# Kernel optimization log

Measured on AMD Instinct MI355X. Metric: run time of the kernel, lower is better.

The kernel has to match this reference:

```python
import jax, jax.numpy as jnp
import numpy as np

B, L, H = 2, 2048, 1024
NH = 4
K = int(H * 0.5)       # key_dim = 512
V = int(H * 1.0)       # value_dim = 1024
DK, DV = K // NH, V // NH   # 128, 256
PR = 32                # proj_low_rank_dim
GR = 64                # gate_low_rank_dim
EPS = 1e-5


def setup_inputs() -> dict:
    key = jax.random.key(0)
    ks = jax.random.split(key, 16)
    s = 0.02
    return {
        "x": jax.random.normal(ks[0], (B, L, H), jnp.float32),
        "mu_x": jax.random.normal(ks[1], (H,), jnp.float32) * s,      # LerpLinear mu of x_proj[0]
        "Wx1": jax.random.normal(ks[2], (5 * PR, H), jnp.float32) * s,  # x_proj[0].linear
        "Wx2": jax.random.normal(ks[3], (H, 5 * PR), jnp.float32) * s,  # x_proj[2]
        "x_bias": jax.random.normal(ks[4], (5, H), jnp.float32) * s,
        "Wr": jax.random.normal(ks[5], (K, H), jnp.float32) * s,
        "Wk": jax.random.normal(ks[6], (K, H), jnp.float32) * s,
        "Wv": jax.random.normal(ks[7], (V, H), jnp.float32) * s,
        "Wg": jax.random.normal(ks[8], (V, H), jnp.float32) * s,
        "Ww1": jax.random.normal(ks[9], (GR, H), jnp.float32) * s,     # w_proj LoRA down
        "Ww2": jax.random.normal(ks[10], (K, GR), jnp.float32) * s,    # w_proj LoRA up
        "bw2": jax.random.normal(ks[11], (K,), jnp.float32) * s,
        "bonus": jax.random.normal(ks[12], (NH, DK), jnp.float32) * s,  # u
        "ln_w": jnp.ones((DV,), jnp.float32),
        "ln_b": jnp.zeros((DV,), jnp.float32),
        "Wo": jax.random.normal(ks[13], (H, V), jnp.float32) * s,
    }


def reference(x, mu_x, Wx1, Wx2, x_bias, Wr, Wk, Wv, Wg, Ww1, Ww2, bw2,
              bonus, ln_w, ln_b, Wo):
    b, l, h = x.shape
    # token shift: shifted[t] = x[t-1], zeros at t=0 (nn.ZeroPad2d((0,0,1,-1)))
    shifted = jnp.pad(x, ((0, 0), (1, 0), (0, 0)))[:, :-1]
    delta = shifted - x

    # x_proj: LerpLinear -> tanh -> einsum with o_proj-like weight, 5 mixing vectors
    xp = jnp.tanh((x + delta * mu_x) @ Wx1.T).reshape(b, l, 5, PR)
    mus = jnp.einsum('blnr,hnr->blnh', xp, Wx2.reshape(H, 5, PR)) + x_bias
    mu_r, mu_w, mu_k, mu_v, mu_g = (mus[:, :, i] for i in range(5))

    # DDLerpLinear projections: linear(x + delta * mu)
    r = (x + delta * mu_r) @ Wr.T                                   # [B,L,K]
    w = jnp.tanh((x + delta * mu_w) @ Ww1.T) @ Ww2.T + bw2          # LoRA, [B,L,K]
    k = (x + delta * mu_k) @ Wk.T                                   # [B,L,K]
    v = (x + delta * mu_v) @ Wv.T                                   # [B,L,V]
    g = (x + delta * mu_g) @ Wg.T                                   # [B,L,V]

    r = r.reshape(b, l, NH, DK)
    k = k.reshape(b, l, NH, DK)
    v = v.reshape(b, l, NH, DV)
    w = -jnp.exp(w.reshape(b, l, NH, DK))   # log-decay (negative)

    def step(S, inp):
        r_t, k_t, v_t, w_t = inp                                    # [B,h,dk]/[B,h,dv]
        kv = k_t[..., :, None] * v_t[..., None, :]                  # [B,h,dk,dv]
        o_t = jnp.einsum('bhk,bhkv->bhv', r_t,
                         S + bonus[None, :, :, None] * kv)
        S = jnp.exp(w_t)[..., None] * S + kv
        return S, o_t

    seq = (r.transpose(1, 0, 2, 3), k.transpose(1, 0, 2, 3),
           v.transpose(1, 0, 2, 3), w.transpose(1, 0, 2, 3))
    S0 = jnp.zeros((b, NH, DK, DV), x.dtype)
    _, o = jax.lax.scan(step, S0, seq)       # [L,B,h,dv]
    o = o.transpose(1, 0, 2, 3)              # [B,L,h,dv]

    # per-head LayerNorm fused with swish gate
    mean = o.mean(-1, keepdims=True)
    var = o.var(-1, keepdims=True)
    o = (o - mean) * jax.lax.rsqrt(var + EPS) * ln_w + ln_b
    gh = g.reshape(b, l, NH, DV)
    o = o * (gh * jax.nn.sigmoid(gh))        # swish gate

    return o.reshape(b, l, V) @ Wo.T         # [B,L,H]
```

## Files before the change

kernel.cpp:

```cpp
#include <hip/hip_runtime.h>
#include <cstdint>
#include <cstddef>

#define H     1024
#define LSEQ  2048
#define NHH   4
#define DKK   128
#define DVV   256
#define KDIM  512
#define VDIM  1024
#define GRR   64
#define MTOT  4096
#define SEGL  128
#define NSEG  16

enum { EPI_NONE = 0, EPI_TANH = 1, EPI_LERP = 2, EPI_DEC = 3, EPI_TANH16 = 4 };

typedef __attribute__((ext_vector_type(8))) _Float16 half8;
typedef __attribute__((ext_vector_type(4))) float f32x4;
typedef __attribute__((ext_vector_type(2))) float f32x2;

static __device__ __forceinline__ unsigned short f2h(float f) {
    _Float16 h = (_Float16)f;
    union { _Float16 h; unsigned short u; } c;
    c.h = h;
    return c.u;
}

template<int CTRL>
static __device__ __forceinline__ float dpp_add(float x) {
    int xi = __float_as_int(x);
    int mv = __builtin_amdgcn_update_dpp(0, xi, CTRL, 0xf, 0xf, true);
    return x + __int_as_float(mv);
}

template<int EPI>
__global__ __launch_bounds__(256) void gemm_bt(
    const float* __restrict__ A, int lda, int acol,
    const float* __restrict__ B, int ldb, int bcol,
    float* __restrict__ Cf, unsigned short* __restrict__ C2, int ldc,
    int M, int N, int K,
    const float* __restrict__ xsrc,
    const float* __restrict__ bias)
{
    if constexpr (EPI == EPI_LERP) {
        const int zz = blockIdx.z;
        acol += zz * 32;
        bcol += zz * 32;
        bias += zz * H;
        C2   += (size_t)zz * 4194304;
    }
    __shared__ float As[16][64];
    __shared__ float Bs[16][64];
    const int m0 = blockIdx.x * 64;
    const int n0 = blockIdx.y * 64;
    const int t  = threadIdx.x;
    const int tx = t & 15, ty = t >> 4;
    const int sm = t >> 2;
    const int sq = (t & 3) * 4;

    float acc[4][4];
#pragma unroll
    for (int i = 0; i < 4; i++)
#pragma unroll
        for (int j = 0; j < 4; j++) acc[i][j] = 0.f;

    for (int k0 = 0; k0 < K; k0 += 16) {
        {
            const int m = m0 + sm;
            const float4 av = *(const float4*)(A + (size_t)m * lda + acol + k0 + sq);
            As[sq + 0][sm] = av.x; As[sq + 1][sm] = av.y;
            As[sq + 2][sm] = av.z; As[sq + 3][sm] = av.w;
        }
        {
            const int n = n0 + sm;
            float4 bv = make_float4(0.f, 0.f, 0.f, 0.f);
            if (n < N) bv = *(const float4*)(B + (size_t)n * ldb + bcol + k0 + sq);
            Bs[sq + 0][sm] = bv.x; Bs[sq + 1][sm] = bv.y;
            Bs[sq + 2][sm] = bv.z; Bs[sq + 3][sm] = bv.w;
        }
        __syncthreads();
#pragma unroll
        for (int kk = 0; kk < 16; kk++) {
            const float4 a = *(const float4*)&As[kk][ty * 4];
            const float4 b = *(const float4*)&Bs[kk][tx * 4];
            const float av2[4] = {a.x, a.y, a.z, a.w};
            const float bv2[4] = {b.x, b.y, b.z, b.w};
#pragma unroll
            for (int i = 0; i < 4; i++)
#pragma unroll
                for (int j = 0; j < 4; j++) acc[i][j] += av2[i] * bv2[j];
        }
        __syncthreads();
    }

    const int nbase = n0 + tx * 4;
    if (nbase >= N) return;
#pragma unroll
    for (int i = 0; i < 4; i++) {
        const int m = m0 + ty * 4 + i;
        float4 r = make_float4(acc[i][0], acc[i][1], acc[i][2], acc[i][3]);
        if constexpr (EPI == EPI_LERP) {
            const float4 bb = *(const float4*)(bias + nbase);
            const float4 xv = *(const float4*)(xsrc + (size_t)m * H + nbase);
            float4 pv = make_float4(0.f, 0.f, 0.f, 0.f);
            if ((m & (LSEQ - 1)) != 0)
                pv = *(const float4*)(xsrc + (size_t)(m - 1) * H + nbase);
            r.x = xv.x + (pv.x - xv.x) * (r.x + bb.x);
            r.y = xv.y + (pv.y - xv.y) * (r.y + bb.y);
            r.z = xv.z + (pv.z - xv.z) * (r.z + bb.z);
            r.w = xv.w + (pv.w - xv.w) * (r.w + bb.w);
        }
        if (Cf) *(float4*)(Cf + (size_t)m * ldc + nbase) = r;
        if (C2) {
            ushort4 p;
            p.x = f2h(r.x); p.y = f2h(r.y); p.z = f2h(r.z); p.w = f2h(r.w);
            *(ushort4*)(C2 + (size_t)m * ldc + nbase) = p;
        }
    }
}

template<int EPI>
__global__ __launch_bounds__(256) void gemm_mfma_bt(
    const unsigned short* __restrict__ A,
    const unsigned short* __restrict__ A2, int nsplit, int lda,
    const unsigned short* __restrict__ B, int ldb,
    float* __restrict__ C, unsigned short* __restrict__ Ch, int ldc, int K,
    const float* __restrict__ bias)
{
    __shared__ __align__(16) unsigned short As[128 * 32];
    __shared__ __align__(16) unsigned short Bs[128 * 32];
    const int t    = threadIdx.x;
    const int w    = t >> 6;
    const int lane = t & 63;
    const int m0 = blockIdx.x * 128;
    const int n0 = blockIdx.y * 128;
    const unsigned short* Au = (n0 < nsplit) ? A : A2;
    const int mw = (w & 1) * 64;
    const int nw = (w >> 1) * 64;
    const int l15 = lane & 15;
    const int q4  = lane >> 4;

    f32x4 acc[4][4];
#pragma unroll
    for (int i = 0; i < 4; i++)
#pragma unroll
        for (int j = 0; j < 4; j++) {
            f32x4 z = {0.f, 0.f, 0.f, 0.f};
            acc[i][j] = z;
        }

    for (int k0 = 0; k0 < K; k0 += 32) {
        __syncthreads();
#pragma unroll
        for (int jj = 0; jj < 2; jj++) {
            const int c   = w * 128 + jj * 64 + lane;
            const int row = c >> 2;
            const int col = (c & 3) * 8;
            __builtin_amdgcn_global_load_lds(
                (const __attribute__((address_space(1))) void*)(Au + (size_t)(m0 + row) * lda + k0 + col),
                (__attribute__((address_space(3))) void*)((char*)As + (w * 128 + jj * 64) * 16),
                16, 0, 0);
            __builtin_amdgcn_global_load_lds(
                (const __attribute__((address_space(1))) void*)(B + (size_t)(n0 + row) * ldb + k0 + col),
                (__attribute__((address_space(3))) void*)((char*)Bs + (w * 128 + jj * 64) * 16),
                16, 0, 0);
        }
        __syncthreads();

        half8 a[4], b[4];
#pragma unroll
        for (int i = 0; i < 4; i++)
            a[i] = *(const half8*)(As + (mw + i * 16 + l15) * 32 + q4 * 8);
#pragma unroll
        for (int j = 0; j < 4; j++)
            b[j] = *(const half8*)(Bs + (nw + j * 16 + l15) * 32 + q4 * 8);
#pragma unroll
        for (int i = 0; i < 4; i++)
#pragma unroll
            for (int j = 0; j < 4; j++)
                acc[i][j] = __builtin_amdgcn_mfma_f32_16x16x32_f16(a[i], b[j], acc[i][j], 0, 0, 0);
    }

#pragma unroll
    for (int i = 0; i < 4; i++) {
        const int m_base = m0 + mw + i * 16 + q4 * 4;
#pragma unroll
        for (int j = 0; j < 4; j++) {
            const int n = n0 + nw + j * 16 + l15;
#pragma unroll
            for (int r = 0; r < 4; r++) {
                float val = acc[i][j][r];
                if constexpr (EPI == EPI_TANH) {
                    C[(size_t)(m_base + r) * ldc + n] = tanhf(val);
                } else if constexpr (EPI == EPI_TANH16) {
                    Ch[(size_t)(m_base + r) * ldc + n] = f2h(tanhf(val));
                } else if constexpr (EPI == EPI_DEC) {
                    C[(size_t)(m_base + r) * ldc + n] = expf(-expf(val + bias[n]));
                } else {
                    C[(size_t)(m_base + r) * ldc + n] = val;
                }
            }
        }
    }
}

__global__ __launch_bounds__(256) void gemm_mfma_corr(
    const unsigned short* __restrict__ rt16,
    const unsigned short* __restrict__ SentryT16,
    float* __restrict__ o)
{
    const int z   = blockIdx.z;
    const int seg = (z >> 3) + 1;
    const int bh  = z & 7;
    const int b   = bh >> 2, h = bh & 3;
    const unsigned short* A = rt16 + ((size_t)b * LSEQ + seg * SEGL) * KDIM + h * DKK;
    const unsigned short* B = SentryT16 + (size_t)(seg * 8 + bh) * 32768;
    float* C = o + ((size_t)b * LSEQ + seg * SEGL) * VDIM + h * DVV;

    __shared__ __align__(16) unsigned short As[128 * 32];
    __shared__ __align__(16) unsigned short Bs[128 * 32];
    const int t    = threadIdx.x;
    const int w    = t >> 6;
    const int lane = t & 63;
    const int m0 = blockIdx.x * 128;
    const int n0 = blockIdx.y * 128;
    const int mw = (w & 1) * 64;
    const int nw = (w >> 1) * 64;
    const int l15 = lane & 15;
    const int q4  = lane >> 4;

    f32x4 acc[4][4];
#pragma unroll
    for (int i = 0; i < 4; i++)
#pragma unroll
        for (int j = 0; j < 4; j++) {
            f32x4 zz = {0.f, 0.f, 0.f, 0.f};
            acc[i][j] = zz;
        }

    for (int k0 = 0; k0 < 128; k0 += 32) {
        __syncthreads();
#pragma unroll
        for (int jj = 0; jj < 2; jj++) {
            const int c   = w * 128 + jj * 64 + lane;
            const int row = c >> 2;
            const int col = (c & 3) * 8;
            __builtin_amdgcn_global_load_lds(
                (const __attribute__((address_space(1))) void*)(A + (size_t)(m0 + row) * KDIM + k0 + col),
                (__attribute__((address_space(3))) void*)((char*)As + (w * 128 + jj * 64) * 16),
                16, 0, 0);
            __builtin_amdgcn_global_load_lds(
                (const __attribute__((address_space(1))) void*)(B + (size_t)(n0 + row) * 128 + k0 + col),
                (__attribute__((address_space(3))) void*)((char*)Bs + (w * 128 + jj * 64) * 16),
                16, 0, 0);
        }
        __syncthreads();

        half8 a[4], bb[4];
#pragma unroll
        for (int i = 0; i < 4; i++)
            a[i] = *(const half8*)(As + (mw + i * 16 + l15) * 32 + q4 * 8);
#pragma unroll
        for (int j = 0; j < 4; j++)
            bb[j] = *(const half8*)(Bs + (nw + j * 16 + l15) * 32 + q4 * 8);
#pragma unroll
        for (int i = 0; i < 4; i++)
#pragma unroll
            for (int j = 0; j < 4; j++)
                acc[i][j] = __builtin_amdgcn_mfma_f32_16x16x32_f16(a[i], bb[j], acc[i][j], 0, 0, 0);
    }

#pragma unroll
    for (int i = 0; i < 4; i++) {
        const int m_base = m0 + mw + i * 16 + q4 * 4;
#pragma unroll
        for (int j = 0; j < 4; j++) {
            const int n = n0 + nw + j * 16 + l15;
#pragma unroll
            for (int rr = 0; rr < 4; rr++)
                C[(size_t)(m_base + rr) * VDIM + n] += acc[i][j][rr];
        }
    }
}

__global__ __launch_bounds__(256) void prep_kernel(
    const float* __restrict__ Wr, const float* __restrict__ Wk,
    const float* __restrict__ Wv, const float* __restrict__ Wg,
    const float* __restrict__ Wo, const float* __restrict__ Wx1,
    const float* __restrict__ Ww1, const float* __restrict__ Ww2,
    unsigned short* __restrict__ Wb, unsigned short* __restrict__ Wx1p,
    unsigned short* __restrict__ Ww1p, unsigned short* __restrict__ Ww2p,
    const float* __restrict__ x, const float* __restrict__ mux,
    unsigned short* __restrict__ xl16)
{
    const int bx = blockIdx.x;
    if (bx < 4512) {
        const int q = bx * 256 + threadIdx.x;
        float4 v = make_float4(0.f, 0.f, 0.f, 0.f);
        unsigned short* dst;
        if (q < 1048576) {
            const int i4 = q * 4;
            const float* src; int off;
            if      (i4 <  524288) { src = Wr; off = i4; }
            else if (i4 < 1048576) { src = Wk; off = i4 -  524288; }
            else if (i4 < 2097152) { src = Wv; off = i4 - 1048576; }
            else if (i4 < 3145728) { src = Wg; off = i4 - 2097152; }
            else                   { src = Wo; off = i4 - 3145728; }
            v = *(const float4*)(src + off);
            dst = Wb + i4;
        } else if (q < 1114112) {
            const int e = (q - 1048576) * 4;
            const int row = e >> 10;
            if (row < 160) v = *(const float4*)(Wx1 + (size_t)row * H + (e & 1023));
            dst = Wx1p + e;
        } else if (q < 1146880) {
            const int e = (q - 1114112) * 4;
            const int row = e >> 10;
            if (row < 64) v = *(const float4*)(Ww1 + (size_t)row * H + (e & 1023));
            dst = Ww1p + e;
        } else {
            const int e = (q - 1146880) * 4;
            v = *(const float4*)(Ww2 + e);
            dst = Ww2p + e;
        }
        ushort4 o4;
        o4.x = f2h(v.x); o4.y = f2h(v.y); o4.z = f2h(v.z); o4.w = f2h(v.w);
        *(ushort4*)dst = o4;
    } else {
        const int m = bx - 4512;
        const int c = threadIdx.x * 4;
        const float4 xv = *(const float4*)(x + (size_t)m * H + c);
        float4 pv = make_float4(0.f, 0.f, 0.f, 0.f);
        if ((m & (LSEQ - 1)) != 0)
            pv = *(const float4*)(x + (size_t)(m - 1) * H + c);
        const float4 mv = *(const float4*)(mux + c);
        ushort4 p;
        p.x = f2h(xv.x + (pv.x - xv.x) * mv.x);
        p.y = f2h(xv.y + (pv.y - xv.y) * mv.y);
        p.z = f2h(xv.z + (pv.z - xv.z) * mv.z);
        p.w = f2h(xv.w + (pv.w - xv.w) * mv.w);
        *(ushort4*)(xl16 + (size_t)m * H + c) = p;
    }
}

__global__ __launch_bounds__(256, 4) void scan_pass1(
    const float* __restrict__ rk, const float* __restrict__ vg,
    const float* __restrict__ dec, const float* __restrict__ bonus,
    float* __restrict__ o, unsigned short* __restrict__ rt16,
    float* __restrict__ Sloc, float* __restrict__ Dtot)
{
    const int bh  = blockIdx.x & 7;
    const int vc  = (blockIdx.x >> 3) & 7;
    const int seg = blockIdx.x >> 6;
    const int b   = bh >> 2;
    const int h   = bh & 3;
    const int t   = threadIdx.x;
    const int kg  = t & 31;
    const int vl  = t >> 5;
    const bool wlead = (vc == 0) && (vl == 0);

    f32x2 S2[4][2];
    float D[4] = {1.f, 1.f, 1.f, 1.f}, u[4];
#pragma unroll
    for (int j = 0; j < 4; j++) {
        u[j] = bonus[h * DKK + kg * 4 + j];
        f32x2 z = {0.f, 0.f};
        S2[j][0] = z; S2[j][1] = z;
    }

    const size_t row0 = (size_t)b * LSEQ + (size_t)seg * SEGL;
    const float* rp = rk  + row0 * 1024 + h * DKK + kg * 4;
    const float* dp = dec + row0 * 512  + h * DKK + kg * 4;
    const float* vp = vg  + row0 * 2048 + h * DVV + vc * 32 + vl * 4;
    float*       op = o   + row0 * 1024 + h * DVV + vc * 32 + vl * 4;
    unsigned short* rt = rt16 + row0 * 512 + h * DKK + kg * 4;

    float4 cr = *(const float4*)rp;
    float4 ck = *(const float4*)(rp + 512);
    float4 cd = *(const float4*)dp;
    float4 cv = *(const float4*)vp;
    rp += 1024; dp += 512; vp += 2048;

    for (int t0 = 0; t0 < SEGL; ++t0) {
        const float4 nr = *(const float4*)rp;
        const float4 nk = *(const float4*)(rp + 512);
        const float4 nd = *(const float4*)dp;
        const float4 nv = *(const float4*)vp;
        rp += 1024; dp += 512; vp += 2048;

        if (wlead) {
            ushort4 p;
            p.x = f2h(cr.x * D[0]); p.y = f2h(cr.y * D[1]);
            p.z = f2h(cr.z * D[2]); p.w = f2h(cr.w * D[3]);
            *(ushort4*)rt = p;
        }
        rt += 512;

        const float ra[4] = {cr.x, cr.y, cr.z, cr.w};
        const float ka[4] = {ck.x, ck.y, ck.z, ck.w};
        const float da[4] = {cd.x, cd.y, cd.z, cd.w};
        f32x2 va2[2];
        va2[0].x = cv.x; va2[0].y = cv.y;
        va2[1].x = cv.z; va2[1].y = cv.w;
        f32x2 part2[2];
        part2[0] = (f32x2){0.f, 0.f};
        part2[1] = (f32x2){0.f, 0.f};
#pragma unroll
        for (int j = 0; j < 4; j++) {
#pragma unroll
            for (int p = 0; p < 2; p++) {
                const f32x2 kv2 = va2[p] * ka[j];
                part2[p] += ra[j] * (S2[j][p] + u[j] * kv2);
                S2[j][p] = da[j] * S2[j][p] + kv2;
            }
            D[j] *= da[j];
        }
        float part[4] = {part2[0].x, part2[0].y, part2[1].x, part2[1].y};
#pragma unroll
        for (int jj = 0; jj < 4; jj++) {
            part[jj] = dpp_add<0xB1>(part[jj]);
            part[jj] = dpp_add<0x4E>(part[jj]);
            part[jj] = dpp_add<0x141>(part[jj]);
            part[jj] = dpp_add<0x140>(part[jj]);
            part[jj] = dpp_add<0x142>(part[jj]);
        }
        if (kg == 31) {
            float4 res = make_float4(part[0], part[1], part[2], part[3]);
            *(float4*)op = res;
        }
        op += 1024;
        cr = nr; ck = nk; cd = nd; cv = nv;
    }

    {
        float* sl = Sloc + (size_t)(seg * 8 + bh) * 32768
                    + (size_t)(kg * 4) * 256 + vc * 32 + vl * 4;
#pragma unroll
        for (int j = 0; j < 4; j++) {
            float4 sv = make_float4(S2[j][0].x, S2[j][0].y, S2[j][1].x, S2[j][1].y);
            *(float4*)(sl + j * 256) = sv;
        }
        if (wlead) {
            float* dt = Dtot + (seg * 8 + bh) * 128 + kg * 4;
#pragma unroll
            for (int j = 0; j < 4; j++) dt[j] = D[j];
        }
    }
}

__global__ __launch_bounds__(256) void scan_pass2(
    const float* __restrict__ Sloc, const float* __restrict__ Dtot,
    unsigned short* __restrict__ SentryT16)
{
    const int vc = blockIdx.x & 31;
    const int bh = blockIdx.x >> 5;
    const int t  = threadIdx.x;
    const int kg = t & 31;
    const int vl = t >> 5;

    float S[4] = {0.f, 0.f, 0.f, 0.f};
    for (int p = 0; p < NSEG; p++) {
        unsigned short* st = SentryT16 + (size_t)(p * 8 + bh) * 32768
                             + (size_t)(vc * 8 + vl) * 128 + kg * 4;
        ushort4 pk;
        pk.x = f2h(S[0]); pk.y = f2h(S[1]); pk.z = f2h(S[2]); pk.w = f2h(S[3]);
        *(ushort4*)st = pk;
        if (p < NSEG - 1) {
            const float* sl = Sloc + (size_t)(p * 8 + bh) * 32768
                              + (size_t)(kg * 4) * 256 + vc * 8 + vl;
            const float* dt = Dtot + (p * 8 + bh) * 128 + kg * 4;
#pragma unroll
            for (int j = 0; j < 4; j++) S[j] = dt[j] * S[j] + sl[j * 256];
        }
    }
}

__global__ __launch_bounds__(256) void ln_gate_kernel(
    const float* __restrict__ o, const float* __restrict__ vg,
    const float* __restrict__ lnw, const float* __restrict__ lnb,
    unsigned short* __restrict__ out)
{
    const int m    = blockIdx.x;
    const int t    = threadIdx.x;
    const int h    = t >> 6;
    const int lane = t & 63;
    const size_t obase = (size_t)m * VDIM + (size_t)h * DVV + lane * 4;
    const size_t gbase = (size_t)m * 2048 + 1024 + (size_t)h * DVV + lane * 4;
    const float4 ov = *(const float4*)(o + obase);
    float sum = ov.x + ov.y + ov.z + ov.w;
    float sq  = ov.x * ov.x + ov.y * ov.y + ov.z * ov.z + ov.w * ov.w;
#pragma unroll
    for (int off = 1; off < 64; off <<= 1) {
        sum += __shfl_xor(sum, off);
        sq  += __shfl_xor(sq, off);
    }
    const float mean = sum * (1.f / DVV);
    const float var  = sq * (1.f / DVV) - mean * mean;
    const float rstd = rsqrtf(var + 1e-5f);
    const float4 gv = *(const float4*)(vg + gbase);
    const float4 wv = *(const float4*)(lnw + lane * 4);
    const float4 bv = *(const float4*)(lnb + lane * 4);
    float4 res;
    res.x = ((ov.x - mean) * rstd * wv.x + bv.x) * (gv.x / (1.f + expf(-gv.x)));
    res.y = ((ov.y - mean) * rstd * wv.y + bv.y) * (gv.y / (1.f + expf(-gv.y)));
    res.z = ((ov.z - mean) * rstd * wv.z + bv.z) * (gv.z / (1.f + expf(-gv.z)));
    res.w = ((ov.w - mean) * rstd * wv.w + bv.w) * (gv.w / (1.f + expf(-gv.w)));
    ushort4 p;
    p.x = f2h(res.x); p.y = f2h(res.y); p.z = f2h(res.z); p.w = f2h(res.w);
    *(ushort4*)(out + obase) = p;
}

extern "C" void kernel_launch(void* const* d_in, const int* in_sizes, int n_in,
                              void* d_out, int out_size, void* d_ws, size_t ws_size,
                              hipStream_t stream)
{
    const float* x     = (const float*)d_in[0];
    const float* mu_x  = (const float*)d_in[1];
    const float* Wx1   = (const float*)d_in[2];
    const float* Wx2   = (const float*)d_in[3];
    const float* xb    = (const float*)d_in[4];
    const float* Wr    = (const float*)d_in[5];
    const float* Wk    = (const float*)d_in[6];
    const float* Wv    = (const float*)d_in[7];
    const float* Wg    = (const float*)d_in[8];
    const float* Ww1   = (const float*)d_in[9];
    const float* Ww2   = (const float*)d_in[10];
    const float* bw2   = (const float*)d_in[11];
    const float* bonus = (const float*)d_in[12];
    const float* lnw   = (const float*)d_in[13];
    const float* lnb   = (const float*)d_in[14];
    const float* Wo    = (const float*)d_in[15];
    float* out = (float*)d_out;
    (void)in_sizes; (void)n_in; (void)out_size; (void)ws_size;

    float* ws = (float*)d_ws;
    unsigned short* Wx1p = (unsigned short*)(ws + 0);
    unsigned short* Ww1p = (unsigned short*)(ws + 131072);
    unsigned short* Ww2p = (unsigned short*)(ws + 196608);
    unsigned short* Wb   = (unsigned short*)(ws + 212992);
    float* xp     = ws + 2310144;
    unsigned short* wlow16 = (unsigned short*)(ws + 3358720);
    float* insB   = ws + 3620864;
    float* rkB    = ws + 14106624;
    float* vgB    = ws + 18301952;
    float* decB   = ws + 26692608;

    unsigned short* insb = (unsigned short*)insB;
    unsigned short* Wrb  = Wb;
    unsigned short* Wvb  = Wb + 1048576;
    unsigned short* Wob  = Wb + 3145728;
    unsigned short* xl16 = (unsigned short*)rkB;
    float*          o       = insB;
    unsigned short* rt16    = insb + 2ul * 4194304;
    float*          Sloc    = insB + 3ul * 2097152;
    float*          Dtot    = (float*)wlow16;
    unsigned short* SentryT16 = (unsigned short*)decB;
    unsigned short* gatedb  = (unsigned short*)(insB + 3ul * 2097152);

    dim3 blk(256);

    prep_kernel<<<dim3(8608), blk, 0, stream>>>(Wr, Wk, Wv, Wg, Wo, Wx1, Ww1, Ww2,
                                                Wb, Wx1p, Ww1p, Ww2p, x, mu_x, xl16);

    gemm_mfma_bt<EPI_TANH><<<dim3(32, 2), blk, 0, stream>>>(
        xl16, xl16, 1 << 30, H, Wx1p, H, xp, nullptr, 256, H, nullptr);

    gemm_bt<EPI_LERP><<<dim3(64, 16, 5), blk, 0, stream>>>(
        xp, 256, 0, Wx2, 160, 0, nullptr, insb, H, MTOT, H, 32, x, xb);

    gemm_mfma_bt<EPI_TANH16><<<dim3(32, 1), blk, 0, stream>>>(
        insb + 1ul * 4194304, insb + 1ul * 4194304, 1 << 30, H, Ww1p, H,
        nullptr, wlow16, 128, H, nullptr);

    gemm_mfma_bt<EPI_DEC><<<dim3(32, 4), blk, 0, stream>>>(
        wlow16, wlow16, 1 << 30, 128, Ww2p, 64, decB, nullptr, KDIM, 64, bw2);

    gemm_mfma_bt<EPI_NONE><<<dim3(32, 8), blk, 0, stream>>>(
        insb + 0ul * 4194304, insb + 2ul * 4194304, 512, H, Wrb, H, rkB, nullptr, 1024, H, nullptr);
    gemm_mfma_bt<EPI_NONE><<<dim3(32, 16), blk, 0, stream>>>(
        insb + 3ul * 4194304, insb + 4ul * 4194304, 1024, H, Wvb, H, vgB, nullptr, 2048, H, nullptr);

    scan_pass1<<<dim3(1024), blk, 0, stream>>>(rkB, vgB, decB, bonus, o, rt16, Sloc, Dtot);
    scan_pass2<<<dim3(256), blk, 0, stream>>>(Sloc, Dtot, SentryT16);
    gemm_mfma_corr<<<dim3(1, 2, 120), blk, 0, stream>>>(rt16, SentryT16, o);

    ln_gate_kernel<<<dim3(4096), blk, 0, stream>>>(o, vgB, lnw, lnb, gatedb);

    gemm_mfma_bt<EPI_NONE><<<dim3(32, 8), blk, 0, stream>>>(
        gatedb, gatedb, 1 << 30, VDIM, Wob, VDIM, out, nullptr, H, VDIM, nullptr);
}
```

Measured before the change: 424.9 us.

## Halve scan segment length, merge projection GEMMs, store segment states in fp16

Shrinks the chunked-scan segment length from 128 to 64, doubling the number of segments and pass-1 blocks, and raises pass-1 occupancy bounds. The three projection GEMMs (r/k, v/g, decay) are merged into one launch with a per-block dispatch, and the correction GEMM is reshaped so each block covers a whole 64x256 segment tile. Per-segment local states are stored in fp16 instead of fp32 to cut traffic into pass 2. The intent is more parallelism, fewer launches and less memory traffic, at the cost of a longer serial pass-2 chain, more correction blocks and reduced state precision.

```diff
diff --git a/kernel.cpp b/kernel.cpp
--- a/kernel.cpp
+++ b/kernel.cpp
@@ -11,8 +11,8 @@
 #define VDIM  1024
 #define GRR   64
 #define MTOT  4096
-#define SEGL  128
-#define NSEG  16
+#define SEGL  64
+#define NSEG  32
 
 enum { EPI_NONE = 0, EPI_TANH = 1, EPI_LERP = 2, EPI_DEC = 3, EPI_TANH16 = 4 };
 
@@ -25,6 +25,11 @@
     union { _Float16 h; unsigned short u; } c;
     c.h = h;
     return c.u;
+}
+static __device__ __forceinline__ float h2f(unsigned short u) {
+    union { unsigned short u; _Float16 h; } c;
+    c.u = u;
+    return (float)c.h;
 }
 
 template<int CTRL>
@@ -195,8 +200,6 @@
                     C[(size_t)(m_base + r) * ldc + n] = tanhf(val);
                 } else if constexpr (EPI == EPI_TANH16) {
                     Ch[(size_t)(m_base + r) * ldc + n] = f2h(tanhf(val));
-                } else if constexpr (EPI == EPI_DEC) {
-                    C[(size_t)(m_base + r) * ldc + n] = expf(-expf(val + bias[n]));
                 } else {
                     C[(size_t)(m_base + r) * ldc + n] = val;
                 }
@@ -205,12 +208,112 @@
     }
 }
 
+__global__ __launch_bounds__(256) void gemm_mfma_mega(
+    const unsigned short* __restrict__ insb,
+    const unsigned short* __restrict__ wlow16,
+    const unsigned short* __restrict__ Ww2p,
+    const unsigned short* __restrict__ Wrb,
+    const unsigned short* __restrict__ Wvb,
+    float* __restrict__ rkB, float* __restrict__ vgB, float* __restrict__ decB,
+    const float* __restrict__ bw2)
+{
+    const int bx = blockIdx.x;
+    const unsigned short *A, *A2, *B;
+    float* C;
+    int nsplit, lda, ldb, ldc, K, epi, local;
+    if (bx < 512) {
+        local = bx;
+        A  = insb + 3ul * 4194304; A2 = insb + 4ul * 4194304;
+        nsplit = 1024; lda = 1024; B = Wvb; ldb = 1024;
+        C = vgB; ldc = 2048; K = 1024; epi = 0;
+    } else if (bx < 768) {
+        local = bx - 512;
+        A  = insb;                 A2 = insb + 2ul * 4194304;
+        nsplit = 512; lda = 1024; B = Wrb; ldb = 1024;
+        C = rkB; ldc = 1024; K = 1024; epi = 0;
+    } else {
+        local = bx - 768;
+        A = wlow16; A2 = wlow16;
+        nsplit = 1 << 30; lda = 128; B = Ww2p; ldb = 64;
+        C = decB; ldc = 512; K = 64; epi = 1;
+    }
+    const int m0 = (local & 31) * 128;
+    const int n0 = (local >> 5) * 128;
+
+    __shared__ __align__(16) unsigned short As[128 * 32];
+    __shared__ __align__(16) unsigned short Bs[128 * 32];
+    const int t    = threadIdx.x;
+    const int w    = t >> 6;
+    const int lane = t & 63;
+    const unsigned short* Au = (n0 < nsplit) ? A : A2;
+    const int mw = (w & 1) * 64;
+    const int nw = (w >> 1) * 64;
+    const int l15 = lane & 15;
+    const int q4  = lane >> 4;
+
+    f32x4 acc[4][4];
+#pragma unroll
+    for (int i = 0; i < 4; i++)
+#pragma unroll
+        for (int j = 0; j < 4; j++) {
+            f32x4 z = {0.f, 0.f, 0.f, 0.f};
+            acc[i][j] = z;
+        }
+
+    for (int k0 = 0; k0 < K; k0 += 32) {
+        __syncthreads();
+#pragma unroll
+        for (int jj = 0; jj < 2; jj++) {
+            const int c   = w * 128 + jj * 64 + lane;
+            const int row = c >> 2;
+            const int col = (c & 3) * 8;
+            __builtin_amdgcn_global_load_lds(
+                (const __attribute__((address_space(1))) void*)(Au + (size_t)(m0 + row) * lda + k0 + col),
+                (__attribute__((address_space(3))) void*)((char*)As + (w * 128 + jj * 64) * 16),
+                16, 0, 0);
+            __builtin_amdgcn_global_load_lds(
+                (const __attribute__((address_space(1))) void*)(B + (size_t)(n0 + row) * ldb + k0 + col),
+                (__attribute__((address_space(3))) void*)((char*)Bs + (w * 128 + jj * 64) * 16),
+                16, 0, 0);
+        }
+        __syncthreads();
+
+        half8 a[4], b[4];
+#pragma unroll
+        for (int i = 0; i < 4; i++)
+            a[i] = *(const half8*)(As + (mw + i * 16 + l15) * 32 + q4 * 8);
+#pragma unroll
+        for (int j = 0; j < 4; j++)
+            b[j] = *(const half8*)(Bs + (nw + j * 16 + l15) * 32 + q4 * 8);
+#pragma unroll
+        for (int i = 0; i < 4; i++)
+#pragma unroll
+            for (int j = 0; j < 4; j++)
+                acc[i][j] = __builtin_amdgcn_mfma_f32_16x16x32_f16(a[i], b[j], acc[i][j], 0, 0, 0);
+    }
+
+#pragma unroll
+    for (int i = 0; i < 4; i++) {
+        const int m_base = m0 + mw + i * 16 + q4 * 4;
+#pragma unroll
+        for (int j = 0; j < 4; j++) {
+            const int n = n0 + nw + j * 16 + l15;
+#pragma unroll
+            for (int r = 0; r < 4; r++) {
+                float val = acc[i][j][r];
+                if (epi) val = expf(-expf(val + bw2[n]));
+                C[(size_t)(m_base + r) * ldc + n] = val;
+            }
+        }
+    }
+}
+
 __global__ __launch_bounds__(256) void gemm_mfma_corr(
     const unsigned short* __restrict__ rt16,
     const unsigned short* __restrict__ SentryT16,
     float* __restrict__ o)
 {
-    const int z   = blockIdx.z;
+    const int z   = blockIdx.x;
     const int seg = (z >> 3) + 1;
     const int bh  = z & 7;
     const int b   = bh >> 2, h = bh & 3;
@@ -218,15 +321,11 @@
     const unsigned short* B = SentryT16 + (size_t)(seg * 8 + bh) * 32768;
     float* C = o + ((size_t)b * LSEQ + seg * SEGL) * VDIM + h * DVV;
 
-    __shared__ __align__(16) unsigned short As[128 * 32];
-    __shared__ __align__(16) unsigned short Bs[128 * 32];
+    __shared__ __align__(16) unsigned short As[64 * 32];
+    __shared__ __align__(16) unsigned short Bs[256 * 32];
     const int t    = threadIdx.x;
     const int w    = t >> 6;
     const int lane = t & 63;
-    const int m0 = blockIdx.x * 128;
-    const int n0 = blockIdx.y * 128;
-    const int mw = (w & 1) * 64;
-    const int nw = (w >> 1) * 64;
     const int l15 = lane & 15;
     const int q4  = lane >> 4;
 
@@ -241,18 +340,23 @@
 
     for (int k0 = 0; k0 < 128; k0 += 32) {
         __syncthreads();
-#pragma unroll
-        for (int jj = 0; jj < 2; jj++) {
-            const int c   = w * 128 + jj * 64 + lane;
+        {
+            const int c   = w * 64 + lane;
             const int row = c >> 2;
             const int col = (c & 3) * 8;
             __builtin_amdgcn_global_load_lds(
-                (const __attribute__((address_space(1))) void*)(A + (size_t)(m0 + row) * KDIM + k0 + col),
-                (__attribute__((address_space(3))) void*)((char*)As + (w * 128 + jj * 64) * 16),
+                (const __attribute__((address_space(1))) void*)(A + (size_t)row * KDIM + k0 + col),
+                (__attribute__((address_space(3))) void*)((char*)As + (w * 64) * 16),
                 16, 0, 0);
+        }
+#pragma unroll
+        for (int jj = 0; jj < 4; jj++) {
+            const int c   = jj * 256 + w * 64 + lane;
+            const int row = c >> 2;
+            const int col = (c & 3) * 8;
             __builtin_amdgcn_global_load_lds(
-                (const __attribute__((address_space(1))) void*)(B + (size_t)(n0 + row) * 128 + k0 + col),
-                (__attribute__((address_space(3))) void*)((char*)Bs + (w * 128 + jj * 64) * 16),
+                (const __attribute__((address_space(1))) void*)(B + (size_t)row * 128 + k0 + col),
+                (__attribute__((address_space(3))) void*)((char*)Bs + (jj * 256 + w * 64) * 16),
                 16, 0, 0);
         }
         __syncthreads();
@@ -260,10 +364,10 @@
         half8 a[4], bb[4];
 #pragma unroll
         for (int i = 0; i < 4; i++)
-            a[i] = *(const half8*)(As + (mw + i * 16 + l15) * 32 + q4 * 8);
+            a[i] = *(const half8*)(As + (i * 16 + l15) * 32 + q4 * 8);
 #pragma unroll
         for (int j = 0; j < 4; j++)
-            bb[j] = *(const half8*)(Bs + (nw + j * 16 + l15) * 32 + q4 * 8);
+            bb[j] = *(const half8*)(Bs + (w * 64 + j * 16 + l15) * 32 + q4 * 8);
 #pragma unroll
         for (int i = 0; i < 4; i++)
 #pragma unroll
@@ -273,10 +377,10 @@
 
 #pragma unroll
     for (int i = 0; i < 4; i++) {
-        const int m_base = m0 + mw + i * 16 + q4 * 4;
-#pragma unroll
-        for (int j = 0; j < 4; j++) {
-            const int n = n0 + nw + j * 16 + l15;
+        const int m_base = i * 16 + q4 * 4;
+#pragma unroll
+        for (int j = 0; j < 4; j++) {
+            const int n = w * 64 + j * 16 + l15;
 #pragma unroll
             for (int rr = 0; rr < 4; rr++)
                 C[(size_t)(m_base + rr) * VDIM + n] += acc[i][j][rr];
@@ -344,11 +448,11 @@
     }
 }
 
-__global__ __launch_bounds__(256, 4) void scan_pass1(
+__global__ __launch_bounds__(256, 8) void scan_pass1(
     const float* __restrict__ rk, const float* __restrict__ vg,
     const float* __restrict__ dec, const float* __restrict__ bonus,
     float* __restrict__ o, unsigned short* __restrict__ rt16,
-    float* __restrict__ Sloc, float* __restrict__ Dtot)
+    unsigned short* __restrict__ Sloc16, float* __restrict__ Dtot)
 {
     const int bh  = blockIdx.x & 7;
     const int vc  = (blockIdx.x >> 3) & 7;
@@ -434,12 +538,14 @@
     }
 
     {
-        float* sl = Sloc + (size_t)(seg * 8 + bh) * 32768
-                    + (size_t)(kg * 4) * 256 + vc * 32 + vl * 4;
-#pragma unroll
-        for (int j = 0; j < 4; j++) {
-            float4 sv = make_float4(S2[j][0].x, S2[j][0].y, S2[j][1].x, S2[j][1].y);
-            *(float4*)(sl + j * 256) = sv;
+        unsigned short* sl16 = Sloc16 + (size_t)(seg * 8 + bh) * 32768
+                               + (size_t)(kg * 4) * 256 + vc * 32 + vl * 4;
+#pragma unroll
+        for (int j = 0; j < 4; j++) {
+            ushort4 sv;
+            sv.x = f2h(S2[j][0].x); sv.y = f2h(S2[j][0].y);
+            sv.z = f2h(S2[j][1].x); sv.w = f2h(S2[j][1].y);
+            *(ushort4*)(sl16 + j * 256) = sv;
         }
         if (wlead) {
             float* dt = Dtot + (seg * 8 + bh) * 128 + kg * 4;
@@ -450,7 +556,7 @@
 }
 
 __global__ __launch_bounds__(256) void scan_pass2(
-    const float* __restrict__ Sloc, const float* __restrict__ Dtot,
+    const unsigned short* __restrict__ Sloc16, const float* __restrict__ Dtot,
     unsigned short* __restrict__ SentryT16)
 {
     const int vc = blockIdx.x & 31;
@@ -467,11 +573,11 @@
         pk.x = f2h(S[0]); pk.y = f2h(S[1]); pk.z = f2h(S[2]); pk.w = f2h(S[3]);
         *(ushort4*)st = pk;
         if (p < NSEG - 1) {
-            const float* sl = Sloc + (size_t)(p * 8 + bh) * 32768
-                              + (size_t)(kg * 4) * 256 + vc * 8 + vl;
+            const unsigned short* sl = Sloc16 + (size_t)(p * 8 + bh) * 32768
+                                       + (size_t)(kg * 4) * 256 + vc * 8 + vl;
             const float* dt = Dtot + (p * 8 + bh) * 128 + kg * 4;
 #pragma unroll
-            for (int j = 0; j < 4; j++) S[j] = dt[j] * S[j] + sl[j * 256];
+            for (int j = 0; j < 4; j++) S[j] = dt[j] * S[j] + h2f(sl[j * 256]);
         }
     }
 }
@@ -553,9 +659,9 @@
     unsigned short* xl16 = (unsigned short*)rkB;
     float*          o       = insB;
     unsigned short* rt16    = insb + 2ul * 4194304;
-    float*          Sloc    = insB + 3ul * 2097152;
+    unsigned short* Sloc16  = insb + 3ul * 4194304;
     float*          Dtot    = (float*)wlow16;
-    unsigned short* SentryT16 = (unsigned short*)decB;
+    unsigned short* SentryT16 = (unsigned short*)rkB;
     unsigned short* gatedb  = (unsigned short*)(insB + 3ul * 2097152);
 
     dim3 blk(256);
@@ -573,17 +679,12 @@
         insb + 1ul * 4194304, insb + 1ul * 4194304, 1 << 30, H, Ww1p, H,
         nullptr, wlow16, 128, H, nullptr);
 
-    gemm_mfma_bt<EPI_DEC><<<dim3(32, 4), blk, 0, stream>>>(
-        wlow16, wlow16, 1 << 30, 128, Ww2p, 64, decB, nullptr, KDIM, 64, bw2);
-
-    gemm_mfma_bt<EPI_NONE><<<dim3(32, 8), blk, 0, stream>>>(
-        insb + 0ul * 4194304, insb + 2ul * 4194304, 512, H, Wrb, H, rkB, nullptr, 1024, H, nullptr);
-    gemm_mfma_bt<EPI_NONE><<<dim3(32, 16), blk, 0, stream>>>(
-        insb + 3ul * 4194304, insb + 4ul * 4194304, 1024, H, Wvb, H, vgB, nullptr, 2048, H, nullptr);
-
-    scan_pass1<<<dim3(1024), blk, 0, stream>>>(rkB, vgB, decB, bonus, o, rt16, Sloc, Dtot);
-    scan_pass2<<<dim3(256), blk, 0, stream>>>(Sloc, Dtot, SentryT16);
-    gemm_mfma_corr<<<dim3(1, 2, 120), blk, 0, stream>>>(rt16, SentryT16, o);
+    gemm_mfma_mega<<<dim3(896), blk, 0, stream>>>(
+        insb, wlow16, Ww2p, Wrb, Wvb, rkB, vgB, decB, bw2);
+
+    scan_pass1<<<dim3(2048), blk, 0, stream>>>(rkB, vgB, decB, bonus, o, rt16, Sloc16, Dtot);
+    scan_pass2<<<dim3(256), blk, 0, stream>>>(Sloc16, Dtot, SentryT16);
+    gemm_mfma_corr<<<dim3(248), blk, 0, stream>>>(rt16, SentryT16, o);
 
     ln_gate_kernel<<<dim3(4096), blk, 0, stream>>>(o, vgB, lnw, lnb, gatedb);
 
```

Measured after the change: 912.2 us. 2.15x slower.
